# Kernel optimization log

Hardware: AMD Instinct MI355X
Metric: run time of the kernel (lower is better)

The kernel has to match this reference:

```python
import jax, jax.numpy as jnp
import numpy as np

H = 1024
NH = 16
HD = H // NH  # 64


def setup_inputs() -> dict:
    key = jax.random.key(0)
    ks = jax.random.split(key, 7)
    s = 1.0 / np.sqrt(H)
    return {
        "hidden_states": jax.random.normal(ks[0], (4, 2048, H), dtype=jnp.float32),
        "Wq": jax.random.normal(ks[1], (H, H), dtype=jnp.float32) * s,
        "bq": jnp.zeros((H,), dtype=jnp.float32),
        "Wk": jax.random.normal(ks[2], (H, H), dtype=jnp.float32) * s,
        "bk": jnp.zeros((H,), dtype=jnp.float32),
        "Wv": jax.random.normal(ks[3], (H, H), dtype=jnp.float32) * s,
        "bv": jnp.zeros((H,), dtype=jnp.float32),
    }


def _split_heads(x):
    # [B,S,H] -> [B,NH,S,HD]
    b, s, _ = x.shape
    return x.reshape(b, s, NH, HD).transpose(0, 2, 1, 3)


def reference(hidden_states, Wq, bq, Wk, bk, Wv, bv):
    q = _split_heads(hidden_states @ Wq + bq)
    k = _split_heads(hidden_states @ Wk + bk)
    v = _split_heads(hidden_states @ Wv + bv)
    scores = jnp.einsum("bhqd,bhkd->bhqk", q, k) / jnp.sqrt(jnp.float32(HD))
    probs = jax.nn.softmax(scores, axis=-1)  # dropout p=0 (eval) -> identity
    ctx = jnp.einsum("bhqk,bhkd->bhqd", probs, v)
    b, _, s, _ = ctx.shape
    return ctx.transpose(0, 2, 1, 3).reshape(b, s, H)
```

## Files before the change

kernel.cpp:

```cpp
#include <hip/hip_runtime.h>
#include <hip/hip_bf16.h>

#define BB  4
#define SS  2048
#define HH  1024
#define NHH 16
#define HDD 64

typedef unsigned short u16;
typedef unsigned int   u32;
using bf16x8 = __attribute__((ext_vector_type(8))) short;
using f32x4  = __attribute__((ext_vector_type(4))) float;

__device__ __forceinline__ u16 f2b(float f) {
    union { float f; u32 u; } x; x.f = f;
    return (u16)((x.u + 0x7fffu + ((x.u >> 16) & 1u)) >> 16);
}
__device__ __forceinline__ u32 pk2b(float lo, float hi) {
    union { float f; u32 u; } a, b; a.f = lo; b.f = hi;
    return __builtin_amdgcn_perm(b.u + 0x8000u, a.u + 0x8000u, 0x07060302u);
}

__device__ __forceinline__ void gload16(const u16* g, u16* l) {
    __builtin_amdgcn_global_load_lds(
        (const __attribute__((address_space(1))) void*)g,
        (__attribute__((address_space(3))) void*)l, 16, 0, 0);
}

__global__ __launch_bounds__(256) void conv(
    const float* __restrict__ X,
    const float* __restrict__ Wq, const float* __restrict__ Wk,
    const float* __restrict__ Wv,
    u16* __restrict__ Xb, u16* __restrict__ Wt)
{
    const int bid = blockIdx.x;
    const int t = threadIdx.x;
    if (bid < 4096) {
        const int i = bid * 256 + t;
        float4 a = ((const float4*)X)[i * 2];
        float4 b = ((const float4*)X)[i * 2 + 1];
        ushort4 s0, s1;
        s0.x = f2b(a.x); s0.y = f2b(a.y); s0.z = f2b(a.z); s0.w = f2b(a.w);
        s1.x = f2b(b.x); s1.y = f2b(b.y); s1.z = f2b(b.z); s1.w = f2b(b.w);
        ((ushort4*)Xb)[i * 2] = s0;
        ((ushort4*)Xb)[i * 2 + 1] = s1;
        return;
    }
    const int idx = bid - 4096;
    const int z = idx >> 10, rem = idx & 1023;
    const int k0 = (rem >> 5) * 32, n0 = (rem & 31) * 32;
    const float* W = (z == 0) ? Wq : (z == 1) ? Wk : Wv;
    u16* out = Wt + (size_t)z * HH * HH;
    __shared__ float T[32][33];
    {
        const int kl = t >> 3, n4 = (t & 7) * 4;
        float4 v = *(const float4*)&W[(size_t)(k0 + kl) * HH + n0 + n4];
        T[n4 + 0][kl] = v.x; T[n4 + 1][kl] = v.y;
        T[n4 + 2][kl] = v.z; T[n4 + 3][kl] = v.w;
    }
    __syncthreads();
    {
        const int nl = t >> 3, k4 = (t & 7) * 4;
        ushort4 s;
        s.x = f2b(T[nl][k4 + 0]); s.y = f2b(T[nl][k4 + 1]);
        s.z = f2b(T[nl][k4 + 2]); s.w = f2b(T[nl][k4 + 3]);
        *(ushort4*)&out[(size_t)(n0 + nl) * HH + k0 + k4] = s;
    }
}

__global__ __launch_bounds__(256) void qkv_gemm(
    const u16* __restrict__ Xb, const u16* __restrict__ Wtb,
    const float* __restrict__ bq, const float* __restrict__ bk,
    const float* __restrict__ bv,
    u16* __restrict__ Qw, u16* __restrict__ Kw, u16* __restrict__ Vw)
{
    const int z  = blockIdx.z;
    const float* bias = (z == 0) ? bq : (z == 1) ? bk : bv;
    const int m0 = blockIdx.x * 128, n0 = blockIdx.y * 128;

    __shared__ __align__(16) u16 Xs[128 * 64];
    __shared__ __align__(16) u16 Ws[128 * 64];

    const int t = threadIdx.x;
    const int w = t >> 6, lane = t & 63, lr = lane & 15, quad = lane >> 4;
    const int l3 = lane >> 3, c7 = lane & 7;
    const int cl = (c7 ^ l3) * 8;
    const int wm = w >> 1, wn = w & 1;

    const u16* Wtz = Wtb + (size_t)z * HH * HH;

    f32x4 acc[4][4];
    #pragma unroll
    for (int i = 0; i < 4; i++)
        #pragma unroll
        for (int j = 0; j < 4; j++) acc[i][j] = f32x4{0.f, 0.f, 0.f, 0.f};

    for (int k0 = 0; k0 < HH; k0 += 64) {
        #pragma unroll
        for (int e = 0; e < 4; e++) {
            const int r = w * 32 + e * 8 + l3;
            gload16(&Xb [(size_t)(m0 + r) * HH + k0 + cl], &Xs[(w * 32 + e * 8) * 64]);
            gload16(&Wtz[(size_t)(n0 + r) * HH + k0 + cl], &Ws[(w * 32 + e * 8) * 64]);
        }
        __syncthreads();

        #pragma unroll
        for (int kc = 0; kc < 2; kc++) {
            bf16x8 af[4], bfr[4];
            const int ph = ((kc * 4 + quad) ^ c7) * 8;
            #pragma unroll
            for (int mi = 0; mi < 4; mi++)
                af[mi] = *(const bf16x8*)&Xs[(wm * 64 + mi * 16 + lr) * 64 + ph];
            #pragma unroll
            for (int ni = 0; ni < 4; ni++)
                bfr[ni] = *(const bf16x8*)&Ws[(wn * 64 + ni * 16 + lr) * 64 + ph];
            if (z != 2) {
                #pragma unroll
                for (int mi = 0; mi < 4; mi++)
                    #pragma unroll
                    for (int ni = 0; ni < 4; ni++)
                        acc[mi][ni] = __builtin_amdgcn_mfma_f32_16x16x32_bf16(
                            bfr[ni], af[mi], acc[mi][ni], 0, 0, 0);
            } else {
                #pragma unroll
                for (int mi = 0; mi < 4; mi++)
                    #pragma unroll
                    for (int ni = 0; ni < 4; ni++)
                        acc[mi][ni] = __builtin_amdgcn_mfma_f32_16x16x32_bf16(
                            af[mi], bfr[ni], acc[mi][ni], 0, 0, 0);
            }
        }
        __syncthreads();
    }

    if (z != 2) {
        u16* dst = (z == 0) ? Qw : Kw;
        const float cs = (z == 0) ? 0.18033688011112042f : 1.0f;
        #pragma unroll
        for (int mi = 0; mi < 4; mi++) {
            const int sg = m0 + wm * 64 + mi * 16 + lr;
            const int b = sg >> 11, s = sg & 2047;
            #pragma unroll
            for (int ni = 0; ni < 4; ni++) {
                const int nb = n0 + wn * 64 + ni * 16 + quad * 4;
                const int h = nb >> 6, d0 = nb & 63;
                float4 bb4 = *(const float4*)&bias[nb];
                ushort4 vs;
                vs.x = f2b((acc[mi][ni][0] + bb4.x) * cs);
                vs.y = f2b((acc[mi][ni][1] + bb4.y) * cs);
                vs.z = f2b((acc[mi][ni][2] + bb4.z) * cs);
                vs.w = f2b((acc[mi][ni][3] + bb4.w) * cs);
                *(ushort4*)&dst[((size_t)(b * NHH + h) * SS + s) * HDD + d0] = vs;
            }
        }
    } else {
        #pragma unroll
        for (int mi = 0; mi < 4; mi++)
            #pragma unroll
            for (int ni = 0; ni < 4; ni++) {
                const int mb = m0 + wm * 64 + mi * 16 + quad * 4;
                const int b = mb >> 11, s0 = mb & 2047;
                const int n = n0 + wn * 64 + ni * 16 + lr;
                const int h = n >> 6, d = n & 63;
                const float bv4 = bias[n];
                ushort4 vs;
                vs.x = f2b(acc[mi][ni][0] + bv4);
                vs.y = f2b(acc[mi][ni][1] + bv4);
                vs.z = f2b(acc[mi][ni][2] + bv4);
                vs.w = f2b(acc[mi][ni][3] + bv4);
                *(ushort4*)&Vw[((size_t)(b * NHH + h) * HDD + d) * SS + s0] = vs;
            }
    }
}

__global__ __launch_bounds__(512) void attn(
    const u16* __restrict__ Qb, const u16* __restrict__ Kb,
    const u16* __restrict__ Vtb, float* __restrict__ Out)
{
    const int bid = blockIdx.x;
    const int hh = bid & 63, qt = bid >> 6;
    const int b = hh >> 4, h = hh & 15;
    const size_t hb = (size_t)hh * SS * HDD;

    __shared__ __align__(16) u16 Ks[2][64 * 64];
    __shared__ __align__(16) u16 Vs[2][64 * 64];
    __shared__ __align__(16) u16 Ps[8][16 * 72];

    const int t = threadIdx.x;
    const int w = t >> 6, lane = t & 63, lr = lane & 15, quad = lane >> 4;
    const int l3 = lane >> 3, c7 = lane & 7;
    const int cl = (c7 ^ l3) * 8;

    bf16x8 qa[2];
    #pragma unroll
    for (int kc = 0; kc < 2; kc++)
        qa[kc] = *(const bf16x8*)&Qb[hb + (size_t)(qt * 128 + w * 16 + lr) * HDD
                                     + kc * 32 + quad * 8];

    {
        const int r8 = w * 8 + l3;
        gload16(&Kb [hb + (size_t)r8 * HDD + cl], &Ks[0][w * 8 * 64]);
        gload16(&Vtb[hb + (size_t)r8 * SS + cl],  &Vs[0][w * 8 * 64]);
    }
    __syncthreads();

    float lsum = 0.f;
    f32x4 oc[4];
    #pragma unroll
    for (int ni = 0; ni < 4; ni++) oc[ni] = f32x4{0.f, 0.f, 0.f, 0.f};

    for (int kt = 0; kt < SS / 64; kt++) {
        const int bb = kt & 1;
        if (kt + 1 < SS / 64) {
            const int r8 = w * 8 + l3;
            gload16(&Kb [hb + (size_t)((kt + 1) * 64 + r8) * HDD + cl],
                    &Ks[bb ^ 1][w * 8 * 64]);
            gload16(&Vtb[hb + (size_t)r8 * SS + (kt + 1) * 64 + cl],
                    &Vs[bb ^ 1][w * 8 * 64]);
        }

        f32x4 sc4[4];
        #pragma unroll
        for (int ni = 0; ni < 4; ni++) sc4[ni] = f32x4{0.f, 0.f, 0.f, 0.f};
        #pragma unroll
        for (int kc = 0; kc < 2; kc++) {
            const int ph = ((kc * 4 + quad) ^ c7) * 8;
            #pragma unroll
            for (int ni = 0; ni < 4; ni++) {
                bf16x8 kf = *(const bf16x8*)&Ks[bb][(ni * 16 + lr) * 64 + ph];
                sc4[ni] = __builtin_amdgcn_mfma_f32_16x16x32_bf16(kf, qa[kc], sc4[ni], 0, 0, 0);
            }
        }

        #pragma unroll
        for (int ni = 0; ni < 4; ni++) {
            float pv0 = __builtin_amdgcn_exp2f(sc4[ni][0]);
            float pv1 = __builtin_amdgcn_exp2f(sc4[ni][1]);
            float pv2 = __builtin_amdgcn_exp2f(sc4[ni][2]);
            float pv3 = __builtin_amdgcn_exp2f(sc4[ni][3]);
            lsum += (pv0 + pv1) + (pv2 + pv3);
            uint2 pk;
            pk.x = pk2b(pv0, pv1);
            pk.y = pk2b(pv2, pv3);
            *(uint2*)&Ps[w][lr * 72 + ni * 16 + quad * 4] = pk;
        }

        bf16x8 pa[2];
        #pragma unroll
        for (int kc = 0; kc < 2; kc++)
            pa[kc] = *(const bf16x8*)&Ps[w][lr * 72 + kc * 32 + quad * 8];

        #pragma unroll
        for (int kc = 0; kc < 2; kc++) {
            const int ph = ((kc * 4 + quad) ^ c7) * 8;
            #pragma unroll
            for (int ni = 0; ni < 4; ni++) {
                bf16x8 vf = *(const bf16x8*)&Vs[bb][(ni * 16 + lr) * 64 + ph];
                oc[ni] = __builtin_amdgcn_mfma_f32_16x16x32_bf16(pa[kc], vf, oc[ni], 0, 0, 0);
            }
        }
        __syncthreads();
    }

    lsum += __shfl_xor(lsum, 16);
    lsum += __shfl_xor(lsum, 32);
    const float linv = 1.0f / lsum;

    #pragma unroll
    for (int ni = 0; ni < 4; ni++)
        #pragma unroll
        for (int r = 0; r < 4; r++) {
            const float inv = __shfl(linv, quad * 4 + r);
            const int rq = qt * 128 + w * 16 + quad * 4 + r;
            Out[((size_t)(b * SS + rq)) * HH + h * HDD + ni * 16 + lr] =
                oc[ni][r] * inv;
        }
}

extern "C" void kernel_launch(void* const* d_in, const int* in_sizes, int n_in,
                              void* d_out, int out_size, void* d_ws, size_t ws_size,
                              hipStream_t stream) {
    const float* X  = (const float*)d_in[0];
    const float* Wq = (const float*)d_in[1];
    const float* bq = (const float*)d_in[2];
    const float* Wk = (const float*)d_in[3];
    const float* bk = (const float*)d_in[4];
    const float* Wv = (const float*)d_in[5];
    const float* bv = (const float*)d_in[6];
    float* Out = (float*)d_out;

    const size_t elems = (size_t)BB * SS * HH;
    u16* Qw = (u16*)d_ws;
    u16* Kw = Qw + elems;
    u16* Vw = Kw + elems;
    u16* Xb = (u16*)d_out;
    u16* Wt = Xb + elems;

    conv<<<dim3(4096 + 3072), 256, 0, stream>>>(X, Wq, Wk, Wv, Xb, Wt);
    qkv_gemm<<<dim3(64, 8, 3), 256, 0, stream>>>(Xb, Wt, bq, bk, bv, Qw, Kw, Vw);
    attn<<<dim3(1024), 512, 0, stream>>>(Qw, Kw, Vw, Out);
}
```

Baseline: 259.2 us.

## Switch attention to 32x32 MFMA with in-register P via permlane swap

```diff
diff --git a/kernel.cpp b/kernel.cpp
--- a/kernel.cpp
+++ b/kernel.cpp
@@ -11,6 +11,8 @@
 typedef unsigned int   u32;
 using bf16x8 = __attribute__((ext_vector_type(8))) short;
 using f32x4  = __attribute__((ext_vector_type(4))) float;
+using f32x16 = __attribute__((ext_vector_type(16))) float;
+using u32x4  = __attribute__((ext_vector_type(4))) u32;
 
 __device__ __forceinline__ u16 f2b(float f) {
     union { float f; u32 u; } x; x.f = f;
@@ -173,7 +175,7 @@
     }
 }
 
-__global__ __launch_bounds__(512) void attn(
+__global__ __launch_bounds__(512, 4) void attn(
     const u16* __restrict__ Qb, const u16* __restrict__ Kb,
     const u16* __restrict__ Vtb, float* __restrict__ Out)
 {
@@ -184,18 +186,20 @@
 
     __shared__ __align__(16) u16 Ks[2][64 * 64];
     __shared__ __align__(16) u16 Vs[2][64 * 64];
-    __shared__ __align__(16) u16 Ps[8][16 * 72];
 
     const int t = threadIdx.x;
-    const int w = t >> 6, lane = t & 63, lr = lane & 15, quad = lane >> 4;
+    const int w = t >> 6, lane = t & 63;
+    const int q32 = lane & 31, hi = lane >> 5;
     const int l3 = lane >> 3, c7 = lane & 7;
     const int cl = (c7 ^ l3) * 8;
 
-    bf16x8 qa[2];
-    #pragma unroll
-    for (int kc = 0; kc < 2; kc++)
-        qa[kc] = *(const bf16x8*)&Qb[hb + (size_t)(qt * 128 + w * 16 + lr) * HDD
-                                     + kc * 32 + quad * 8];
+    bf16x8 qf[4];
+    {
+        const size_t qrow = (size_t)(qt * 256 + w * 32 + q32);
+        #pragma unroll
+        for (int ds = 0; ds < 4; ds++)
+            qf[ds] = *(const bf16x8*)&Qb[hb + qrow * HDD + ds * 16 + hi * 8];
+    }
 
     {
         const int r8 = w * 8 + l3;
@@ -205,9 +209,7 @@
     __syncthreads();
 
     float lsum = 0.f;
-    f32x4 oc[4];
-    #pragma unroll
-    for (int ni = 0; ni < 4; ni++) oc[ni] = f32x4{0.f, 0.f, 0.f, 0.f};
+    f32x16 oc0 = {}, oc1 = {};
 
     for (int kt = 0; kt < SS / 64; kt++) {
         const int bb = kt & 1;
@@ -219,62 +221,71 @@
                     &Vs[bb ^ 1][w * 8 * 64]);
         }
 
-        f32x4 sc4[4];
-        #pragma unroll
-        for (int ni = 0; ni < 4; ni++) sc4[ni] = f32x4{0.f, 0.f, 0.f, 0.f};
-        #pragma unroll
-        for (int kc = 0; kc < 2; kc++) {
-            const int ph = ((kc * 4 + quad) ^ c7) * 8;
-            #pragma unroll
-            for (int ni = 0; ni < 4; ni++) {
-                bf16x8 kf = *(const bf16x8*)&Ks[bb][(ni * 16 + lr) * 64 + ph];
-                sc4[ni] = __builtin_amdgcn_mfma_f32_16x16x32_bf16(kf, qa[kc], sc4[ni], 0, 0, 0);
-            }
-        }
-
-        #pragma unroll
-        for (int ni = 0; ni < 4; ni++) {
-            float pv0 = __builtin_amdgcn_exp2f(sc4[ni][0]);
-            float pv1 = __builtin_amdgcn_exp2f(sc4[ni][1]);
-            float pv2 = __builtin_amdgcn_exp2f(sc4[ni][2]);
-            float pv3 = __builtin_amdgcn_exp2f(sc4[ni][3]);
-            lsum += (pv0 + pv1) + (pv2 + pv3);
-            uint2 pk;
-            pk.x = pk2b(pv0, pv1);
-            pk.y = pk2b(pv2, pv3);
-            *(uint2*)&Ps[w][lr * 72 + ni * 16 + quad * 4] = pk;
-        }
-
-        bf16x8 pa[2];
-        #pragma unroll
-        for (int kc = 0; kc < 2; kc++)
-            pa[kc] = *(const bf16x8*)&Ps[w][lr * 72 + kc * 32 + quad * 8];
-
-        #pragma unroll
-        for (int kc = 0; kc < 2; kc++) {
-            const int ph = ((kc * 4 + quad) ^ c7) * 8;
-            #pragma unroll
-            for (int ni = 0; ni < 4; ni++) {
-                bf16x8 vf = *(const bf16x8*)&Vs[bb][(ni * 16 + lr) * 64 + ph];
-                oc[ni] = __builtin_amdgcn_mfma_f32_16x16x32_bf16(pa[kc], vf, oc[ni], 0, 0, 0);
-            }
-        }
+        f32x16 sc0 = {}, sc1 = {};
+        __builtin_amdgcn_s_setprio(1);
+        #pragma unroll
+        for (int ds = 0; ds < 4; ds++) {
+            const int ph = ((ds * 2 + hi) ^ c7) * 8;
+            bf16x8 kf0 = *(const bf16x8*)&Ks[bb][q32 * 64 + ph];
+            bf16x8 kf1 = *(const bf16x8*)&Ks[bb][(32 + q32) * 64 + ph];
+            sc0 = __builtin_amdgcn_mfma_f32_32x32x16_bf16(kf0, qf[ds], sc0, 0, 0, 0);
+            sc1 = __builtin_amdgcn_mfma_f32_32x32x16_bf16(kf1, qf[ds], sc1, 0, 0, 0);
+        }
+        __builtin_amdgcn_s_setprio(0);
+
+        union PU { u32x4 u; bf16x8 v; } pa[4];
+        #pragma unroll
+        for (int kb = 0; kb < 2; kb++) {
+            const f32x16 s = kb ? sc1 : sc0;
+            float p[16];
+            #pragma unroll
+            for (int r = 0; r < 16; r++) p[r] = __builtin_amdgcn_exp2f(s[r]);
+            lsum += ((((p[0] + p[1]) + (p[2] + p[3]))
+                    + ((p[4] + p[5]) + (p[6] + p[7])))
+                   + (((p[8] + p[9]) + (p[10] + p[11]))
+                    + ((p[12] + p[13]) + (p[14] + p[15]))));
+            u32 x0, x1, x2, x3, y0, y1, y2, y3;
+            asm("v_cvt_pk_bf16_f32 %0, %1, %2" : "=v"(x0) : "v"(p[0]),  "v"(p[1]));
+            asm("v_cvt_pk_bf16_f32 %0, %1, %2" : "=v"(x1) : "v"(p[2]),  "v"(p[3]));
+            asm("v_cvt_pk_bf16_f32 %0, %1, %2" : "=v"(y0) : "v"(p[4]),  "v"(p[5]));
+            asm("v_cvt_pk_bf16_f32 %0, %1, %2" : "=v"(y1) : "v"(p[6]),  "v"(p[7]));
+            asm("v_cvt_pk_bf16_f32 %0, %1, %2" : "=v"(x2) : "v"(p[8]),  "v"(p[9]));
+            asm("v_cvt_pk_bf16_f32 %0, %1, %2" : "=v"(x3) : "v"(p[10]), "v"(p[11]));
+            asm("v_cvt_pk_bf16_f32 %0, %1, %2" : "=v"(y2) : "v"(p[12]), "v"(p[13]));
+            asm("v_cvt_pk_bf16_f32 %0, %1, %2" : "=v"(y3) : "v"(p[14]), "v"(p[15]));
+            asm("v_permlane32_swap_b32 %0, %1" : "+v"(x0), "+v"(y0));
+            asm("v_permlane32_swap_b32 %0, %1" : "+v"(x1), "+v"(y1));
+            asm("v_permlane32_swap_b32 %0, %1" : "+v"(x2), "+v"(y2));
+            asm("v_permlane32_swap_b32 %0, %1" : "+v"(x3), "+v"(y3));
+            pa[kb * 2 + 0].u = u32x4{x0, x1, y0, y1};
+            pa[kb * 2 + 1].u = u32x4{x2, x3, y2, y3};
+        }
+
+        __builtin_amdgcn_s_setprio(1);
+        #pragma unroll
+        for (int ks = 0; ks < 4; ks++) {
+            const int ph = ((ks * 2 + hi) ^ c7) * 8;
+            bf16x8 vf0 = *(const bf16x8*)&Vs[bb][q32 * 64 + ph];
+            bf16x8 vf1 = *(const bf16x8*)&Vs[bb][(32 + q32) * 64 + ph];
+            oc0 = __builtin_amdgcn_mfma_f32_32x32x16_bf16(pa[ks].v, vf0, oc0, 0, 0, 0);
+            oc1 = __builtin_amdgcn_mfma_f32_32x32x16_bf16(pa[ks].v, vf1, oc1, 0, 0, 0);
+        }
+        __builtin_amdgcn_s_setprio(0);
         __syncthreads();
     }
 
-    lsum += __shfl_xor(lsum, 16);
     lsum += __shfl_xor(lsum, 32);
     const float linv = 1.0f / lsum;
 
     #pragma unroll
-    for (int ni = 0; ni < 4; ni++)
-        #pragma unroll
-        for (int r = 0; r < 4; r++) {
-            const float inv = __shfl(linv, quad * 4 + r);
-            const int rq = qt * 128 + w * 16 + quad * 4 + r;
-            Out[((size_t)(b * SS + rq)) * HH + h * HDD + ni * 16 + lr] =
-                oc[ni][r] * inv;
-        }
+    for (int r = 0; r < 16; r++) {
+        const int cr = (r & 3) + 8 * (r >> 2) + 4 * hi;
+        const float inv = __shfl(linv, cr);
+        const int rq = qt * 256 + w * 32 + cr;
+        float* o = &Out[((size_t)(b * SS + rq)) * HH + h * HDD + q32];
+        o[0]  = oc0[r] * inv;
+        o[32] = oc1[r] * inv;
+    }
 }
 
 extern "C" void kernel_launch(void* const* d_in, const int* in_sizes, int n_in,
@@ -298,5 +309,5 @@
 
     conv<<<dim3(4096 + 3072), 256, 0, stream>>>(X, Wq, Wk, Wv, Xb, Wt);
     qkv_gemm<<<dim3(64, 8, 3), 256, 0, stream>>>(Xb, Wt, bq, bk, bv, Qw, Kw, Vw);
-    attn<<<dim3(1024), 512, 0, stream>>>(Qw, Kw, Vw, Out);
-}
+    attn<<<dim3(512), 512, 0, stream>>>(Qw, Kw, Vw, Out);
+}
```

After: 238.1 us. -8.1%, faster.
